# Performance work log

Hardware: AMD Instinct MI355X
Metric: run time of the kernel (lower is better)

The kernel has to match this reference:

```python
import jax, jax.numpy as jnp
import numpy as np

N, D, H, C = 16384, 2048, 512, 65
EPS_LOG = 1e-6   # matches torch log(p + 1e-6)
EPS_NORM = 1e-12 # matches F.normalize default eps


def setup_inputs() -> dict:
    key = jax.random.key(0)
    k0, k1, k2 = jax.random.split(key, 3)
    return {
        "feat": jax.random.normal(k0, (N, D), jnp.float32),
        "w1": jax.random.normal(k1, (D, H), jnp.float32) * (1.0 / np.sqrt(D)),
        "b1": jnp.zeros((H,), jnp.float32),
        "w2": jax.random.normal(k2, (H, C), jnp.float32) * (1.0 / np.sqrt(H)),
        "b2": jnp.zeros((C,), jnp.float32),
    }


def reference(feat, w1, b1, w2, b2):
    n, c = feat.shape[0], w2.shape[1]
    # fc1 -> relu -> dropout(p=0.5, training=True; fixed key for determinism) -> fc2
    h = jax.nn.relu(feat @ w1 + b1)
    keep = jax.random.bernoulli(jax.random.key(42), 0.5, h.shape)
    h = jnp.where(keep, h * 2.0, 0.0)
    logits = h @ w2 + b2

    logp = jax.nn.log_softmax(logits, axis=1)
    p = jnp.exp(logp)  # softmax_out

    entropy = -jnp.mean(jnp.sum(p * jnp.log(p + EPS_LOG), axis=1))
    mean_p = jnp.mean(p, axis=0)
    diversity = jnp.sum(mean_p * jnp.log(mean_p + EPS_LOG))

    # per-class centroids: one-pass segment reduce instead of python loop over classes
    pseudo_preds = jnp.argmax(p, axis=1)
    sums = jax.ops.segment_sum(feat, pseudo_preds, num_segments=c)          # [C, D]
    counts = jax.ops.segment_sum(jnp.ones((n,), feat.dtype), pseudo_preds, num_segments=c)
    means = sums / jnp.maximum(counts, 1.0)[:, None]
    norms = jnp.linalg.norm(means, axis=1, keepdims=True)
    centroids = jnp.where(counts[:, None] > 0, means / jnp.maximum(norms, EPS_NORM), 0.0)

    feat_n = feat / jnp.maximum(jnp.linalg.norm(feat, axis=1, keepdims=True), EPS_NORM)
    sim = feat_n @ centroids.T                                              # [N, C]
    pseudo_labels = jnp.argmax(sim, axis=1)

    ce = -jnp.mean(jnp.take_along_axis(logp, pseudo_labels[:, None], axis=1))
    loss = entropy + diversity + 0.3 * ce
    return loss
```

## Files before the change

kernel.cpp:

```cpp
#include <hip/hip_runtime.h>

typedef unsigned short us;
typedef unsigned int u32;
typedef __attribute__((ext_vector_type(8))) short short8;
typedef __attribute__((ext_vector_type(4))) float f32x4;

#define MFMA16(a, b, c) __builtin_amdgcn_mfma_f32_16x16x32_bf16((a), (b), (c), 0, 0, 0)

#define GLD16(lptr, gptr) __builtin_amdgcn_global_load_lds( \
    (__attribute__((address_space(1))) void*)(gptr), \
    (__attribute__((address_space(3))) void*)(lptr), 16, 0, 0)

__device__ inline us f2bf(float f) {
  u32 u = __float_as_uint(f);
  u32 r = (u + 0x7FFFu + ((u >> 16) & 1u)) >> 16;
  return (us)r;
}
__device__ inline float bf2f(us s) { return __uint_as_float((u32)s << 16); }
__device__ inline void splitbf(float x, us& hi, us& lo) {
  hi = f2bf(x);
  lo = f2bf(x - bf2f(hi));
}

#define TF_R(a) { x0 += x1; x1 = (x1 << (a)) | (x1 >> (32 - (a))); x1 ^= x0; }
__global__ __launch_bounds__(256) void k_prep(
    const float* __restrict__ feat, const float* __restrict__ w1, const float* __restrict__ w2,
    us* __restrict__ xh, us* __restrict__ xl,
    us* __restrict__ w1h, us* __restrict__ w1l,
    us* __restrict__ w2h, us* __restrict__ w2l,
    u32* __restrict__ mask, float* __restrict__ accs,
    int* __restrict__ cnt, int* __restrict__ cursor, int* __restrict__ done) {
  __shared__ float tile[64][65];
  int b = blockIdx.x, t = threadIdx.x;
  if (b < 16384) {
    size_t g = ((size_t)b * 256 + t) * 8;
    f32x4 a = *(const f32x4*)(feat + g);
    f32x4 bb = *(const f32x4*)(feat + g + 4);
    short8 h8, l8;
    for (int i = 0; i < 4; ++i) {
      us hi, lo;
      splitbf(a[i], hi, lo); h8[i] = (short)hi; l8[i] = (short)lo;
      splitbf(bb[i], hi, lo); h8[4 + i] = (short)hi; l8[4 + i] = (short)lo;
    }
    *(short8*)(xh + g) = h8;
    *(short8*)(xl + g) = l8;
  } else if (b < 16896) {
    u32 tt = (u32)(b - 16384) * 256u + (u32)t;
    const u32 K0 = 0u, K1 = 42u, K2 = 0x1BD11BDAu ^ 0u ^ 42u;
    u32 w0 = 0, w1r = 0;
    for (int i = 0; i < 32; ++i) {
      u32 x0 = tt * 32u + (u32)i;
      u32 x1 = x0 + 4194304u;
      x0 += K0; x1 += K1;
      TF_R(13) TF_R(15) TF_R(26) TF_R(6)   x0 += K1; x1 += K2 + 1u;
      TF_R(17) TF_R(29) TF_R(16) TF_R(24)  x0 += K2; x1 += K0 + 2u;
      TF_R(13) TF_R(15) TF_R(26) TF_R(6)   x0 += K0; x1 += K1 + 3u;
      TF_R(17) TF_R(29) TF_R(16) TF_R(24)  x0 += K1; x1 += K2 + 4u;
      TF_R(13) TF_R(15) TF_R(26) TF_R(6)   x0 += K2; x1 += K0 + 5u;
      w0 |= (u32)((x0 >> 31) == 0u) << i;
      w1r |= (u32)((x1 >> 31) == 0u) << i;
    }
    mask[tt] = w0;
    mask[tt + 131072u] = w1r;
  } else if (b < 17152) {
    int i = b - 16896;
    int k0 = (i & 31) * 64, n0 = (i >> 5) * 64;
    int cr = t >> 6, cc = t & 63;
    for (int j = 0; j < 16; ++j) {
      int r = j * 4 + cr;
      tile[r][cc] = w1[(size_t)(k0 + r) * 512 + n0 + cc];
    }
    __syncthreads();
    for (int j = 0; j < 16; ++j) {
      int n = j * 4 + cr;
      int k = cc;
      us hi, lo; splitbf(tile[k][n], hi, lo);
      size_t o = (size_t)(n0 + n) * 2048 + k0 + k;
      w1h[o] = hi; w1l[o] = lo;
    }
  } else if (b < 17232) {
    int n = b - 17152;
    for (int k = t; k < 512; k += 256) {
      float v = (n < 65) ? w2[(size_t)k * 65 + n] : 0.f;
      us hi, lo; splitbf(v, hi, lo);
      w2h[n * 512 + k] = hi; w2l[n * 512 + k] = lo;
    }
  } else {
    if (t < 68) accs[t] = 0.f;
    if (t < 65) { cnt[t] = 0; cursor[t] = 0; }
    if (t == 0) done[0] = 0;
  }
}

__global__ __launch_bounds__(256, 2) void k_gemm1(
    const us* __restrict__ Ah_, const us* __restrict__ Al_,
    const us* __restrict__ Bh_, const us* __restrict__ Bl_,
    const float* __restrict__ b1, const u32* __restrict__ mask,
    us* __restrict__ Hh, us* __restrict__ Hl) {
  __shared__ __align__(16) us lds[4 * 8192];
  us* sAh = lds; us* sAl = lds + 8192; us* sBh = lds + 16384; us* sBl = lds + 24576;
  int tid = threadIdx.x;
  int bm = blockIdx.x, bn = blockIdx.y;
  int m0 = bm * 128, n0 = bn * 128;
  int lane = tid & 63, wv = tid >> 6;
  int wm = (wv >> 1) * 64, wn = (wv & 1) * 64;
  int frow = lane & 15, fq = lane >> 4;
  int srow = tid >> 3;
  int scolsw = (((tid & 7) ^ ((tid >> 3) & 7)) * 8);
  f32x4 acc[4][4] = {};
  size_t arow = (size_t)(m0 + srow) * 2048 + scolsw;
  size_t brow = (size_t)(n0 + srow) * 2048 + scolsw;
  for (int kt = 0; kt < 32; ++kt) {
    int k0 = kt * 64;
    __syncthreads();
#pragma unroll
    for (int j = 0; j < 4; ++j) {
      int lo = j * 2048 + wv * 512;
      size_t go = (size_t)j * 32 * 2048 + k0;
      GLD16(sAh + lo, Ah_ + arow + go);
      GLD16(sAl + lo, Al_ + arow + go);
      GLD16(sBh + lo, Bh_ + brow + go);
      GLD16(sBl + lo, Bl_ + brow + go);
    }
    __syncthreads();
#pragma unroll
    for (int s = 0; s < 2; ++s) {
      short8 ah[4], al[4], bh[4], bl[4];
#pragma unroll
      for (int f = 0; f < 4; ++f) {
        int ca = ((s * 4 + fq) ^ (frow & 7)) * 8;
        int ra = (wm + f * 16 + frow) * 64 + ca;
        int rb = (wn + f * 16 + frow) * 64 + ca;
        ah[f] = *(const short8*)&sAh[ra];
        al[f] = *(const short8*)&sAl[ra];
        bh[f] = *(const short8*)&sBh[rb];
        bl[f] = *(const short8*)&sBl[rb];
      }
#pragma unroll
      for (int i = 0; i < 4; ++i)
#pragma unroll
        for (int j2 = 0; j2 < 4; ++j2) {
          acc[i][j2] = MFMA16(ah[i], bh[j2], acc[i][j2]);
          acc[i][j2] = MFMA16(ah[i], bl[j2], acc[i][j2]);
          acc[i][j2] = MFMA16(al[i], bh[j2], acc[i][j2]);
        }
    }
  }
#pragma unroll
  for (int i = 0; i < 4; ++i)
#pragma unroll
    for (int j = 0; j < 4; ++j)
#pragma unroll
      for (int r = 0; r < 4; ++r) {
        int row = m0 + wm + i * 16 + (lane >> 4) * 4 + r;
        int col = n0 + wn + j * 16 + (lane & 15);
        float v = acc[i][j][r] + b1[col];
        v = fmaxf(v, 0.f);
        u32 f = (u32)row * 512u + (u32)col;
        u32 keep = (mask[f >> 5] >> (f & 31u)) & 1u;
        v = keep ? v * 2.f : 0.f;
        us hi, lo; splitbf(v, hi, lo);
        size_t o = (size_t)row * 512 + col;
        Hh[o] = hi; Hl[o] = lo;
      }
}

__global__ __launch_bounds__(256, 2) void k_gemm2(
    const us* __restrict__ Ah_, const us* __restrict__ Al_,
    const us* __restrict__ Bh_, const us* __restrict__ Bl_,
    const float* __restrict__ b2,
    float* __restrict__ logp, int* __restrict__ preds,
    float* __restrict__ accs , int* __restrict__ cnt) {
  __shared__ __align__(16) us sA[2][4096];
  __shared__ __align__(16) us sB[2][5120];
  __shared__ float slog[64 * 81];
  __shared__ float sm[64], sl[64];
  __shared__ float sred[256];
  __shared__ int hh[65];
  int tid = threadIdx.x;
  int m0 = blockIdx.x * 64;
  int lane = tid & 63, wv = tid >> 6;
  int frow = lane & 15, fq = lane >> 4;
  int srow = tid >> 3;
  int scolsw = (((tid & 7) ^ ((tid >> 3) & 7)) * 8);
  f32x4 acc[5] = {};
  size_t arow = (size_t)(m0 + srow) * 512 + scolsw;
  size_t brow = (size_t)srow * 512 + scolsw;
  size_t brow2 = (size_t)(64 + (tid >> 3)) * 512 + scolsw;
  for (int kt = 0; kt < 8; ++kt) {
    int k0 = kt * 64;
    __syncthreads();
#pragma unroll
    for (int j = 0; j < 2; ++j) {
      int lo = j * 2048 + wv * 512;
      size_t go = (size_t)j * 32 * 512 + k0;
      GLD16(&sA[0][lo], Ah_ + arow + go);
      GLD16(&sA[1][lo], Al_ + arow + go);
      GLD16(&sB[0][lo], Bh_ + brow + go);
      GLD16(&sB[1][lo], Bl_ + brow + go);
    }
    if (wv < 2) {
      GLD16(&sB[0][4096 + wv * 512], Bh_ + brow2 + k0);
      GLD16(&sB[1][4096 + wv * 512], Bl_ + brow2 + k0);
    }
    __syncthreads();
#pragma unroll
    for (int s = 0; s < 2; ++s) {
      int ca = ((s * 4 + fq) ^ (frow & 7)) * 8;
      short8 a_h = *(const short8*)&sA[0][(wv * 16 + frow) * 64 + ca];
      short8 a_l = *(const short8*)&sA[1][(wv * 16 + frow) * 64 + ca];
#pragma unroll
      for (int fn = 0; fn < 5; ++fn) {
        short8 b_h = *(const short8*)&sB[0][(fn * 16 + frow) * 64 + ca];
        short8 b_l = *(const short8*)&sB[1][(fn * 16 + frow) * 64 + ca];
        acc[fn] = MFMA16(a_h, b_h, acc[fn]);
        acc[fn] = MFMA16(a_h, b_l, acc[fn]);
        acc[fn] = MFMA16(a_l, b_h, acc[fn]);
      }
    }
  }
#pragma unroll
  for (int fn = 0; fn < 5; ++fn) {
    int col = fn * 16 + (lane & 15);
    if (col < 65) {
      float bb = b2[col];
#pragma unroll
      for (int r = 0; r < 4; ++r) {
        int row = wv * 16 + (lane >> 4) * 4 + r;
        slog[row * 81 + col] = acc[fn][r] + bb;
      }
    }
  }
  if (tid < 65) hh[tid] = 0;
  __syncthreads();
  if (tid < 64) {
    int row = tid;
    float m = -1e30f; int am = 0;
    for (int c = 0; c < 65; ++c) {
      float v = slog[row * 81 + c];
      if (v > m) { m = v; am = c; }
    }
    float s = 0.f;
    for (int c = 0; c < 65; ++c) s += expf(slog[row * 81 + c] - m);
    sm[row] = m; sl[row] = logf(s);
    preds[m0 + row] = am;
    atomicAdd(&hh[am], 1);
  }
  __syncthreads();
  if (tid < 65 && hh[tid] > 0) atomicAdd(&cnt[tid], hh[tid]);
  float entp = 0.f;
  if (tid < 240) {
    int c = tid % 80, rr0 = tid / 80;
    if (c < 65) {
      float mpp = 0.f;
      for (int r = rr0; r < 64; r += 3) {
        float v = slog[r * 81 + c] - sm[r] - sl[r];
        logp[(size_t)(m0 + r) * 65 + c] = v;
        float p = expf(v);
        mpp += p;
        entp += p * logf(p + 1e-6f);
      }
      atomicAdd(&accs[2 + c], mpp);
    }
  }
  sred[tid] = entp;
  __syncthreads();
  for (int s = 128; s > 0; s >>= 1) { if (tid < s) sred[tid] += sred[tid + s]; __syncthreads(); }
  if (tid == 0) atomicAdd(&accs[0], sred[0]);
}

__global__ __launch_bounds__(256) void k_scatter(
    const int* __restrict__ preds, const int* __restrict__ cnt,
    int* __restrict__ cursor, int* __restrict__ rowidx) {
  __shared__ int h[65];
  __shared__ int gb[65];
  __shared__ int sbase[65];
  int tid = threadIdx.x;
  if (tid < 65) { h[tid] = 0; sbase[tid] = cnt[tid]; }
  __syncthreads();
  int i = blockIdx.x * 256 + tid;
  int c = preds[i];
  int pos = atomicAdd(&h[c], 1);
  if (tid == 0) {
    int s = 0;
    for (int cc = 0; cc < 65; ++cc) { int v = sbase[cc]; sbase[cc] = s; s += v; }
  }
  __syncthreads();
  if (tid < 65 && h[tid] > 0) gb[tid] = atomicAdd(&cursor[tid], h[tid]);
  __syncthreads();
  rowidx[sbase[c] + gb[c] + pos] = i;
}

__global__ __launch_bounds__(256) void k_segsum2(
    const float* __restrict__ feat, const int* __restrict__ rowidx,
    const int* __restrict__ cnt,
    float* __restrict__ psum ) {
  int c = blockIdx.x;
  int j = blockIdx.y;
  int tid = threadIdx.x;
  int start = 0;
  for (int cc = 0; cc < 65; ++cc) { if (cc == c) break; start += cnt[cc]; }
  int n = cnt[c];
  f32x4 a0 = {}, a1 = {};
  const float* fp = feat + (size_t)tid * 8;
  for (int i = j; i < n; i += 8) {
    int row = rowidx[start + i];
    const f32x4* p = (const f32x4*)(fp + (size_t)row * 2048);
    a0 += p[0];
    a1 += p[1];
  }
  float* o = psum + ((size_t)(j * 65 + c)) * 2048 + (size_t)tid * 8;
  *(f32x4*)o = a0;
  *(f32x4*)(o + 4) = a1;
}

__global__ __launch_bounds__(256) void k_centroid(
    const float* __restrict__ psum, const int* __restrict__ pcnt,
    us* __restrict__ ch, us* __restrict__ cl) {
  int c = blockIdx.x;
  int tid = threadIdx.x;
  if (c >= 65) {
    for (int d = tid; d < 2048; d += 256) { ch[(size_t)c * 2048 + d] = 0; cl[(size_t)c * 2048 + d] = 0; }
    return;
  }
  int cnt = pcnt[c];
  float inv = 1.0f / (float)((cnt > 1) ? cnt : 1);
  float mean[8]; float sq = 0.f;
  for (int i = 0; i < 8; ++i) {
    int d = tid + i * 256;
    float s = 0.f;
    for (int nc = 0; nc < 8; ++nc) s += psum[((size_t)nc * 65 + c) * 2048 + d];
    mean[i] = s * inv;
    sq += mean[i] * mean[i];
  }
  __shared__ float red[256];
  red[tid] = sq; __syncthreads();
  for (int s = 128; s > 0; s >>= 1) { if (tid < s) red[tid] += red[tid + s]; __syncthreads(); }
  float norm = sqrtf(red[0]);
  float dscale = (cnt > 0) ? 1.0f / fmaxf(norm, 1e-12f) : 0.0f;
  for (int i = 0; i < 8; ++i) {
    int d = tid + i * 256;
    us hi, lo; splitbf(mean[i] * dscale, hi, lo);
    ch[(size_t)c * 2048 + d] = hi; cl[(size_t)c * 2048 + d] = lo;
  }
}

__global__ __launch_bounds__(256, 2) void k_sim(
    const us* __restrict__ Ah_, const us* __restrict__ Al_,
    const us* __restrict__ Bh_, const us* __restrict__ Bl_,
    float* __restrict__ simbuf ) {
  __shared__ __align__(16) us sA[2][4096];
  __shared__ __align__(16) us sB[2][5120];
  int tid = threadIdx.x;
  int m0 = blockIdx.x * 64;
  int ks = blockIdx.y;
  int kbase = ks * 1024;
  int lane = tid & 63, wv = tid >> 6;
  int frow = lane & 15, fq = lane >> 4;
  int srow = tid >> 3;
  int scolsw = (((tid & 7) ^ ((tid >> 3) & 7)) * 8);
  f32x4 acc[5] = {};
  size_t arow = (size_t)(m0 + srow) * 2048 + kbase + scolsw;
  size_t brow = (size_t)srow * 2048 + kbase + scolsw;
  size_t brow2 = (size_t)(64 + (tid >> 3)) * 2048 + kbase + scolsw;
  for (int kt = 0; kt < 16; ++kt) {
    int k0 = kt * 64;
    __syncthreads();
#pragma unroll
    for (int j = 0; j < 2; ++j) {
      int lo = j * 2048 + wv * 512;
      size_t go = (size_t)j * 32 * 2048 + k0;
      GLD16(&sA[0][lo], Ah_ + arow + go);
      GLD16(&sA[1][lo], Al_ + arow + go);
      GLD16(&sB[0][lo], Bh_ + brow + go);
      GLD16(&sB[1][lo], Bl_ + brow + go);
    }
    if (wv < 2) {
      GLD16(&sB[0][4096 + wv * 512], Bh_ + brow2 + k0);
      GLD16(&sB[1][4096 + wv * 512], Bl_ + brow2 + k0);
    }
    __syncthreads();
#pragma unroll
    for (int s = 0; s < 2; ++s) {
      int ca = ((s * 4 + fq) ^ (frow & 7)) * 8;
      short8 a_h = *(const short8*)&sA[0][(wv * 16 + frow) * 64 + ca];
      short8 a_l = *(const short8*)&sA[1][(wv * 16 + frow) * 64 + ca];
#pragma unroll
      for (int fn = 0; fn < 5; ++fn) {
        short8 b_h = *(const short8*)&sB[0][(fn * 16 + frow) * 64 + ca];
        short8 b_l = *(const short8*)&sB[1][(fn * 16 + frow) * 64 + ca];
        acc[fn] = MFMA16(a_h, b_h, acc[fn]);
        acc[fn] = MFMA16(a_h, b_l, acc[fn]);
        acc[fn] = MFMA16(a_l, b_h, acc[fn]);
      }
    }
  }
#pragma unroll
  for (int fn = 0; fn < 5; ++fn) {
    int col = fn * 16 + (lane & 15);
#pragma unroll
    for (int r = 0; r < 4; ++r) {
      int row = wv * 16 + (lane >> 4) * 4 + r;
      simbuf[((size_t)(ks * 16384 + m0 + row)) * 80 + col] = acc[fn][r];
    }
  }
}

__global__ __launch_bounds__(256) void k_simred(
    const float* __restrict__ simbuf, const float* __restrict__ logp,
    float* __restrict__ accs, int* __restrict__ done, float* __restrict__ out) {
  __shared__ float sred[256];
  __shared__ int lastflag;
  int tid = threadIdx.x;
  int row = blockIdx.x * 256 + tid;
  const float* p0 = simbuf + (size_t)row * 80;
  const float* p1 = simbuf + (size_t)(16384 + row) * 80;
  float m = -1e30f; int am = 0;
  for (int c = 0; c < 65; ++c) {
    float v = p0[c] + p1[c];
    if (v > m) { m = v; am = c; }
  }
  sred[tid] = logp[(size_t)row * 65 + am];
  __syncthreads();
  for (int s = 128; s > 0; s >>= 1) { if (tid < s) sred[tid] += sred[tid + s]; __syncthreads(); }
  if (tid == 0) {
    atomicAdd(&accs[1], sred[0]);
    __threadfence();
    int old = atomicAdd(done, 1);
    lastflag = (old == 63);
  }
  __syncthreads();
  if (!lastflag) return;
  float d = 0.f;
  if (tid < 65) {
    float mp = atomicAdd(&accs[2 + tid], 0.f) * (1.f / 16384.f);
    d = mp * logf(mp + 1e-6f);
  }
  sred[tid] = d;
  __syncthreads();
  for (int s = 128; s > 0; s >>= 1) { if (tid < s) sred[tid] += sred[tid + s]; __syncthreads(); }
  if (tid == 0) {
    float entropy = -atomicAdd(&accs[0], 0.f) * (1.f / 16384.f);
    float ce = -atomicAdd(&accs[1], 0.f) * (1.f / 16384.f);
    out[0] = entropy + sred[0] + 0.3f * ce;
  }
}

extern "C" void kernel_launch(void* const* d_in, const int* in_sizes, int n_in,
                              void* d_out, int out_size, void* d_ws, size_t ws_size,
                              hipStream_t stream) {
  const float* feat = (const float*)d_in[0];
  const float* w1   = (const float*)d_in[1];
  const float* b1   = (const float*)d_in[2];
  const float* w2   = (const float*)d_in[3];
  const float* b2   = (const float*)d_in[4];
  float* out = (float*)d_out;

  char* w = (char*)d_ws;
  auto alloc = [&](size_t b) { char* p = w; w += (b + 255) & ~(size_t)255; return p; };
  us*  feat_hi = (us*)alloc(16384ull * 2048 * 2);
  us*  feat_lo = (us*)alloc(16384ull * 2048 * 2);
  us*  w1t_hi  = (us*)alloc(512ull * 2048 * 2);
  us*  w1t_lo  = (us*)alloc(512ull * 2048 * 2);
  us*  w2t_hi  = (us*)alloc(80ull * 512 * 2);
  us*  w2t_lo  = (us*)alloc(80ull * 512 * 2);
  u32* mask    = (u32*)alloc(262144ull * 4);
  us*  h_hi    = (us*)alloc(16384ull * 512 * 2);
  us*  h_lo    = (us*)alloc(16384ull * 512 * 2);
  float* logp  = (float*)alloc(16384ull * 65 * 4);
  int*   preds = (int*)alloc(16384ull * 4);
  float* psum  = (float*)alloc(8ull * 65 * 2048 * 4);
  int*   cnt   = (int*)alloc(65ull * 4);
  int*   cursor= (int*)alloc(65ull * 4);
  int*   rowidx= (int*)alloc(16384ull * 4);
  us*  cent_hi = (us*)alloc(80ull * 2048 * 2);
  us*  cent_lo = (us*)alloc(80ull * 2048 * 2);
  float* simbuf= (float*)alloc(2ull * 16384 * 80 * 4);
  float* accs  = (float*)alloc(68ull * 4);
  int*   done  = (int*)alloc(4ull);

  k_prep<<<17233, 256, 0, stream>>>(feat, w1, w2, feat_hi, feat_lo,
                                    w1t_hi, w1t_lo, w2t_hi, w2t_lo,
                                    mask, accs, cnt, cursor, done);
  k_gemm1<<<dim3(128, 4), 256, 0, stream>>>(feat_hi, feat_lo, w1t_hi, w1t_lo, b1, mask, h_hi, h_lo);
  k_gemm2<<<256, 256, 0, stream>>>(h_hi, h_lo, w2t_hi, w2t_lo, b2, logp, preds, accs, cnt);
  k_scatter<<<64, 256, 0, stream>>>(preds, cnt, cursor, rowidx);
  k_segsum2<<<dim3(65, 8), 256, 0, stream>>>(feat, rowidx, cnt, psum);
  k_centroid<<<80, 256, 0, stream>>>(psum, cnt, cent_hi, cent_lo);
  k_sim<<<dim3(256, 2), 256, 0, stream>>>(feat_hi, feat_lo, cent_hi, cent_lo, simbuf);
  k_simred<<<64, 256, 0, stream>>>(simbuf, logp, accs, done, out);
}
```

Before: 486.3 us.

## Fuse fc2 into fc1 epilogue via LDS tile, add split-K partial logits

The first GEMM's epilogue now stages its activated, dropout-masked hidden tile in shared memory as bf16 hi/lo and multiplies it directly by the matching slice of w2. Each column block writes partial logits to a 4-way buffer. The hidden activation is no longer written to or read back from global memory, and the separate fc2 kernel is removed. A lighter softmax kernel sums the four partials. The segment-sum and similarity kernels also double their split factors (16 segment chunks, 4 K-splits) for more parallelism, at the cost of larger partial buffers and extra reduction reads.

Result: no change. 478.6 us (-1.6%).

```diff
diff --git a/kernel.cpp b/kernel.cpp
--- a/kernel.cpp
+++ b/kernel.cpp
@@ -96,7 +96,8 @@
     const us* __restrict__ Ah_, const us* __restrict__ Al_,
     const us* __restrict__ Bh_, const us* __restrict__ Bl_,
     const float* __restrict__ b1, const u32* __restrict__ mask,
-    us* __restrict__ Hh, us* __restrict__ Hl) {
+    const us* __restrict__ W2h_, const us* __restrict__ W2l_,
+    float* __restrict__ logitsP ) {
   __shared__ __align__(16) us lds[4 * 8192];
   us* sAh = lds; us* sAl = lds + 8192; us* sBh = lds + 16384; us* sBl = lds + 24576;
   int tid = threadIdx.x;
@@ -105,6 +106,7 @@
   int lane = tid & 63, wv = tid >> 6;
   int wm = (wv >> 1) * 64, wn = (wv & 1) * 64;
   int frow = lane & 15, fq = lane >> 4;
+  int quad = lane >> 4;
   int srow = tid >> 3;
   int scolsw = (((tid & 7) ^ ((tid >> 3) & 7)) * 8);
   f32x4 acc[4][4] = {};
@@ -146,89 +148,92 @@
         }
     }
   }
+  __syncthreads();
+  us* sHh = lds;
+  us* sHl = lds + 16384;
 #pragma unroll
   for (int i = 0; i < 4; ++i)
 #pragma unroll
     for (int j = 0; j < 4; ++j)
 #pragma unroll
       for (int r = 0; r < 4; ++r) {
-        int row = m0 + wm + i * 16 + (lane >> 4) * 4 + r;
-        int col = n0 + wn + j * 16 + (lane & 15);
-        float v = acc[i][j][r] + b1[col];
+        int row = wm + i * 16 + quad * 4 + r;
+        int colL = wn + j * 16 + (lane & 15);
+        float v = acc[i][j][r] + b1[n0 + colL];
         v = fmaxf(v, 0.f);
-        u32 f = (u32)row * 512u + (u32)col;
+        u32 f = (u32)(m0 + row) * 512u + (u32)(n0 + colL);
         u32 keep = (mask[f >> 5] >> (f & 31u)) & 1u;
         v = keep ? v * 2.f : 0.f;
         us hi, lo; splitbf(v, hi, lo);
-        size_t o = (size_t)row * 512 + col;
-        Hh[o] = hi; Hl[o] = lo;
-      }
-}
-
-__global__ __launch_bounds__(256, 2) void k_gemm2(
-    const us* __restrict__ Ah_, const us* __restrict__ Al_,
-    const us* __restrict__ Bh_, const us* __restrict__ Bl_,
-    const float* __restrict__ b2,
+        int slab = colL >> 6, k2 = colL & 63;
+        int chunk = ((k2 >> 3) ^ (row & 7));
+        int a = slab * 8192 + row * 64 + chunk * 8 + (k2 & 7);
+        sHh[a] = hi; sHl[a] = lo;
+      }
+  __syncthreads();
+  int wm2 = wv * 32;
+  f32x4 accm[2][5] = {};
+#pragma unroll
+  for (int ks = 0; ks < 4; ++ks) {
+    int slab = ks >> 1;
+    short8 a_h[2], a_l[2];
+#pragma unroll
+    for (int mf = 0; mf < 2; ++mf) {
+      int crow = wm2 + mf * 16 + frow;
+      int cm = ((((ks & 1) * 4 + fq) ^ (frow & 7))) * 8;
+      int a = slab * 8192 + crow * 64 + cm;
+      a_h[mf] = *(const short8*)&sHh[a];
+      a_l[mf] = *(const short8*)&sHl[a];
+    }
+#pragma unroll
+    for (int fn = 0; fn < 5; ++fn) {
+      int c = fn * 16 + frow;
+      size_t bo = (size_t)c * 512 + n0 + ks * 32 + fq * 8;
+      short8 b_h = *(const short8*)(W2h_ + bo);
+      short8 b_l = *(const short8*)(W2l_ + bo);
+#pragma unroll
+      for (int mf = 0; mf < 2; ++mf) {
+        accm[mf][fn] = MFMA16(a_h[mf], b_h, accm[mf][fn]);
+        accm[mf][fn] = MFMA16(a_h[mf], b_l, accm[mf][fn]);
+        accm[mf][fn] = MFMA16(a_l[mf], b_h, accm[mf][fn]);
+      }
+    }
+  }
+#pragma unroll
+  for (int mf = 0; mf < 2; ++mf)
+#pragma unroll
+    for (int fn = 0; fn < 5; ++fn)
+#pragma unroll
+      for (int r = 0; r < 4; ++r) {
+        int grow = m0 + wm2 + mf * 16 + quad * 4 + r;
+        int c = fn * 16 + (lane & 15);
+        logitsP[((size_t)bn * 16384 + grow) * 80 + c] = accm[mf][fn][r];
+      }
+}
+
+__global__ __launch_bounds__(256) void k_softmax(
+    const float* __restrict__ logitsP, const float* __restrict__ b2,
     float* __restrict__ logp, int* __restrict__ preds,
     float* __restrict__ accs , int* __restrict__ cnt) {
-  __shared__ __align__(16) us sA[2][4096];
-  __shared__ __align__(16) us sB[2][5120];
   __shared__ float slog[64 * 81];
   __shared__ float sm[64], sl[64];
   __shared__ float sred[256];
   __shared__ int hh[65];
   int tid = threadIdx.x;
   int m0 = blockIdx.x * 64;
-  int lane = tid & 63, wv = tid >> 6;
-  int frow = lane & 15, fq = lane >> 4;
-  int srow = tid >> 3;
-  int scolsw = (((tid & 7) ^ ((tid >> 3) & 7)) * 8);
-  f32x4 acc[5] = {};
-  size_t arow = (size_t)(m0 + srow) * 512 + scolsw;
-  size_t brow = (size_t)srow * 512 + scolsw;
-  size_t brow2 = (size_t)(64 + (tid >> 3)) * 512 + scolsw;
-  for (int kt = 0; kt < 8; ++kt) {
-    int k0 = kt * 64;
-    __syncthreads();
-#pragma unroll
-    for (int j = 0; j < 2; ++j) {
-      int lo = j * 2048 + wv * 512;
-      size_t go = (size_t)j * 32 * 512 + k0;
-      GLD16(&sA[0][lo], Ah_ + arow + go);
-      GLD16(&sA[1][lo], Al_ + arow + go);
-      GLD16(&sB[0][lo], Bh_ + brow + go);
-      GLD16(&sB[1][lo], Bl_ + brow + go);
-    }
-    if (wv < 2) {
-      GLD16(&sB[0][4096 + wv * 512], Bh_ + brow2 + k0);
-      GLD16(&sB[1][4096 + wv * 512], Bl_ + brow2 + k0);
-    }
-    __syncthreads();
-#pragma unroll
-    for (int s = 0; s < 2; ++s) {
-      int ca = ((s * 4 + fq) ^ (frow & 7)) * 8;
-      short8 a_h = *(const short8*)&sA[0][(wv * 16 + frow) * 64 + ca];
-      short8 a_l = *(const short8*)&sA[1][(wv * 16 + frow) * 64 + ca];
-#pragma unroll
-      for (int fn = 0; fn < 5; ++fn) {
-        short8 b_h = *(const short8*)&sB[0][(fn * 16 + frow) * 64 + ca];
-        short8 b_l = *(const short8*)&sB[1][(fn * 16 + frow) * 64 + ca];
-        acc[fn] = MFMA16(a_h, b_h, acc[fn]);
-        acc[fn] = MFMA16(a_h, b_l, acc[fn]);
-        acc[fn] = MFMA16(a_l, b_h, acc[fn]);
-      }
-    }
-  }
-#pragma unroll
-  for (int fn = 0; fn < 5; ++fn) {
-    int col = fn * 16 + (lane & 15);
-    if (col < 65) {
-      float bb = b2[col];
-#pragma unroll
-      for (int r = 0; r < 4; ++r) {
-        int row = wv * 16 + (lane >> 4) * 4 + r;
-        slog[row * 81 + col] = acc[fn][r] + bb;
-      }
+  int r = tid >> 2, cg = tid & 3;
+  const float* p0 = logitsP + (size_t)(m0 + r) * 80;
+#pragma unroll
+  for (int cc = 0; cc < 5; ++cc) {
+    int c = cg * 20 + cc * 4;
+    f32x4 v = *(const f32x4*)(p0 + c);
+    v += *(const f32x4*)(p0 + 16384ull * 80 + c);
+    v += *(const f32x4*)(p0 + 2ull * 16384 * 80 + c);
+    v += *(const f32x4*)(p0 + 3ull * 16384 * 80 + c);
+#pragma unroll
+    for (int e = 0; e < 4; ++e) {
+      int c2 = c + e;
+      if (c2 < 65) slog[r * 81 + c2] = v[e] + b2[c2];
     }
   }
   if (tid < 65) hh[tid] = 0;
@@ -253,9 +258,9 @@
     int c = tid % 80, rr0 = tid / 80;
     if (c < 65) {
       float mpp = 0.f;
-      for (int r = rr0; r < 64; r += 3) {
-        float v = slog[r * 81 + c] - sm[r] - sl[r];
-        logp[(size_t)(m0 + r) * 65 + c] = v;
+      for (int rr = rr0; rr < 64; rr += 3) {
+        float v = slog[rr * 81 + c] - sm[rr] - sl[rr];
+        logp[(size_t)(m0 + rr) * 65 + c] = v;
         float p = expf(v);
         mpp += p;
         entp += p * logf(p + 1e-6f);
@@ -303,7 +308,7 @@
   int n = cnt[c];
   f32x4 a0 = {}, a1 = {};
   const float* fp = feat + (size_t)tid * 8;
-  for (int i = j; i < n; i += 8) {
+  for (int i = j; i < n; i += 16) {
     int row = rowidx[start + i];
     const f32x4* p = (const f32x4*)(fp + (size_t)row * 2048);
     a0 += p[0];
@@ -329,7 +334,7 @@
   for (int i = 0; i < 8; ++i) {
     int d = tid + i * 256;
     float s = 0.f;
-    for (int nc = 0; nc < 8; ++nc) s += psum[((size_t)nc * 65 + c) * 2048 + d];
+    for (int nc = 0; nc < 16; ++nc) s += psum[((size_t)nc * 65 + c) * 2048 + d];
     mean[i] = s * inv;
     sq += mean[i] * mean[i];
   }
@@ -354,7 +359,7 @@
   int tid = threadIdx.x;
   int m0 = blockIdx.x * 64;
   int ks = blockIdx.y;
-  int kbase = ks * 1024;
+  int kbase = ks * 512;
   int lane = tid & 63, wv = tid >> 6;
   int frow = lane & 15, fq = lane >> 4;
   int srow = tid >> 3;
@@ -363,7 +368,7 @@
   size_t arow = (size_t)(m0 + srow) * 2048 + kbase + scolsw;
   size_t brow = (size_t)srow * 2048 + kbase + scolsw;
   size_t brow2 = (size_t)(64 + (tid >> 3)) * 2048 + kbase + scolsw;
-  for (int kt = 0; kt < 16; ++kt) {
+  for (int kt = 0; kt < 8; ++kt) {
     int k0 = kt * 64;
     __syncthreads();
 #pragma unroll
@@ -414,10 +419,9 @@
   int tid = threadIdx.x;
   int row = blockIdx.x * 256 + tid;
   const float* p0 = simbuf + (size_t)row * 80;
-  const float* p1 = simbuf + (size_t)(16384 + row) * 80;
   float m = -1e30f; int am = 0;
   for (int c = 0; c < 65; ++c) {
-    float v = p0[c] + p1[c];
+    float v = p0[c] + p0[16384ull * 80 + c] + p0[2ull * 16384 * 80 + c] + p0[3ull * 16384 * 80 + c];
     if (v > m) { m = v; am = c; }
   }
   sred[tid] = logp[(size_t)row * 65 + am];
@@ -465,28 +469,28 @@
   us*  w2t_hi  = (us*)alloc(80ull * 512 * 2);
   us*  w2t_lo  = (us*)alloc(80ull * 512 * 2);
   u32* mask    = (u32*)alloc(262144ull * 4);
-  us*  h_hi    = (us*)alloc(16384ull * 512 * 2);
-  us*  h_lo    = (us*)alloc(16384ull * 512 * 2);
+  float* logitsP = (float*)alloc(4ull * 16384 * 80 * 4);
   float* logp  = (float*)alloc(16384ull * 65 * 4);
   int*   preds = (int*)alloc(16384ull * 4);
-  float* psum  = (float*)alloc(8ull * 65 * 2048 * 4);
+  float* psum  = (float*)alloc(16ull * 65 * 2048 * 4);
   int*   cnt   = (int*)alloc(65ull * 4);
   int*   cursor= (int*)alloc(65ull * 4);
   int*   rowidx= (int*)alloc(16384ull * 4);
   us*  cent_hi = (us*)alloc(80ull * 2048 * 2);
   us*  cent_lo = (us*)alloc(80ull * 2048 * 2);
-  float* simbuf= (float*)alloc(2ull * 16384 * 80 * 4);
+  float* simbuf= (float*)alloc(4ull * 16384 * 80 * 4);
   float* accs  = (float*)alloc(68ull * 4);
   int*   done  = (int*)alloc(4ull);
 
   k_prep<<<17233, 256, 0, stream>>>(feat, w1, w2, feat_hi, feat_lo,
                                     w1t_hi, w1t_lo, w2t_hi, w2t_lo,
                                     mask, accs, cnt, cursor, done);
-  k_gemm1<<<dim3(128, 4), 256, 0, stream>>>(feat_hi, feat_lo, w1t_hi, w1t_lo, b1, mask, h_hi, h_lo);
-  k_gemm2<<<256, 256, 0, stream>>>(h_hi, h_lo, w2t_hi, w2t_lo, b2, logp, preds, accs, cnt);
+  k_gemm1<<<dim3(128, 4), 256, 0, stream>>>(feat_hi, feat_lo, w1t_hi, w1t_lo, b1, mask,
+                                            w2t_hi, w2t_lo, logitsP);
+  k_softmax<<<256, 256, 0, stream>>>(logitsP, b2, logp, preds, accs, cnt);
   k_scatter<<<64, 256, 0, stream>>>(preds, cnt, cursor, rowidx);
-  k_segsum2<<<dim3(65, 8), 256, 0, stream>>>(feat, rowidx, cnt, psum);
+  k_segsum2<<<dim3(65, 16), 256, 0, stream>>>(feat, rowidx, cnt, psum);
   k_centroid<<<80, 256, 0, stream>>>(psum, cnt, cent_hi, cent_lo);
-  k_sim<<<dim3(256, 2), 256, 0, stream>>>(feat_hi, feat_lo, cent_hi, cent_lo, simbuf);
+  k_sim<<<dim3(256, 4), 256, 0, stream>>>(feat_hi, feat_lo, cent_hi, cent_lo, simbuf);
   k_simred<<<64, 256, 0, stream>>>(simbuf, logp, accs, done, out);
 }
```
